# Kernel tuning notes

Hardware: AMD Instinct MI355X
Metric: run time of the kernel (lower is better)

Reference implementation:

```python
import jax, jax.numpy as jnp
import numpy as np

HEADS = 8

def setup_inputs() -> dict:
    key = jax.random.key(0)
    ks = jax.random.split(key, 10)
    B, C, D, W, H = 4, 256, 12, 12, 12
    dk = C // HEADS
    return {
        "x": jax.random.normal(ks[0], (B, C, D, W, H), jnp.float32),
        "wq": jax.random.normal(ks[1], (C, C), jnp.float32) * 0.05,
        "bq": jax.random.normal(ks[2], (C,), jnp.float32) * 0.05,
        "wk": jax.random.normal(ks[3], (C, C), jnp.float32) * 0.05,
        "bk": jax.random.normal(ks[4], (C,), jnp.float32) * 0.05,
        "wv": jax.random.normal(ks[5], (C, C), jnp.float32) * 0.05,
        "bv": jax.random.normal(ks[6], (C,), jnp.float32) * 0.05,
        "rel_d": jax.random.normal(ks[7], (1, HEADS, dk, D, 1, 1), jnp.float32),
        "rel_h": jax.random.normal(ks[8], (1, HEADS, dk, 1, 1, H), jnp.float32),
        "rel_w": jax.random.normal(ks[9], (1, HEADS, dk, 1, W, 1), jnp.float32),
    }


def reference(x, wq, bq, wk, bk, wv, bv, rel_d, rel_h, rel_w):
    B, C, D, W, H = x.shape
    dk = C // HEADS
    N = D * W * H

    def proj(w, b):
        # Conv3d kernel_size=1 == per-voxel linear over channels
        y = jnp.einsum('bcdwh,oc->bodwh', x, w) + b[None, :, None, None, None]
        return y.reshape(B, HEADS, dk, N)  # [B,h,dk,N]

    q = proj(wq, bq)
    k = proj(wk, bk)
    v = proj(wv, bv)

    # content-content: q^T k -> [B,h,N,N]
    cc = jnp.einsum('bhdn,bhdm->bhnm', q, k)
    # relative-position bias: (rel_h+rel_w+rel_d) broadcasts to [1,h,dk,D,W,H]
    pos = (rel_h + rel_w + rel_d).reshape(1, HEADS, dk, N)
    # content-position: pos^T @ q -> [B,h,N,N]
    cp = jnp.einsum('bhdn,bhdm->bhnm', pos, q)

    attn = jax.nn.softmax(cc + cp, axis=-1)  # [B,h,N,N]
    # out = v @ attn^T -> [B,h,dk,N]
    out = jnp.einsum('bhdn,bhmn->bhdm', v, attn)
    return out.reshape(B, C, D, W, H)
```

## Files before the change

### kernel.cpp

```cpp
#include <hip/hip_runtime.h>
#include <math.h>

#define HEADS 8
#define DK 32
#define B_ 4
#define C_ 256
#define NVOX 1728
#define DE 64
#define XPITCH 136
#define CPITCH 36
#define LOG2E 1.44269504088896f
#define JSPLIT 3
#define NJT 9
#define ITILES 14

typedef _Float16 f16x8 __attribute__((ext_vector_type(8)));
typedef __fp16 fp16x2 __attribute__((ext_vector_type(2)));
typedef float f32x16 __attribute__((ext_vector_type(16)));

__device__ inline float h2f(short s) {
    _Float16 h = *(_Float16*)&s;
    return (float)h;
}
__device__ inline f32x16 mfma32h(f16x8 a, f16x8 b, f32x16 c) {
    return __builtin_amdgcn_mfma_f32_32x32x16_f16(a, b, c, 0, 0, 0);
}
__device__ __forceinline__ void gl_lds16(const short* g, short* l) {
    __builtin_amdgcn_global_load_lds(
        (const __attribute__((address_space(1))) unsigned int*)g,
        (__attribute__((address_space(3))) unsigned int*)l, 16, 0, 0);
}

union H8 { _Float16 h[8]; uint4 v; };
union H4 { _Float16 h[4]; uint2 v; };
union PW { fp16x2 h2; unsigned int u; };

__global__ __launch_bounds__(256)
void prep_kernel(const float* __restrict__ x,
                 const float* __restrict__ wq, const float* __restrict__ wk,
                 const float* __restrict__ wv,
                 const float* __restrict__ rel_d, const float* __restrict__ rel_h,
                 const float* __restrict__ rel_w,
                 short* __restrict__ wf, short* __restrict__ xf,
                 short* __restrict__ Qf) {
    __shared__ float tile[64][65];
    int bid = blockIdx.x;
    int t = threadIdx.x;

    if (bid < 192) {
        int idx = (bid * 256 + t) * 4;
        int m = idx >> 16;
        const float* w = (m == 0) ? wq : (m == 1) ? wk : wv;
        float4 v = *(const float4*)&w[idx & 65535];
        H4 hh;
        hh.h[0] = (_Float16)v.x; hh.h[1] = (_Float16)v.y;
        hh.h[2] = (_Float16)v.z; hh.h[3] = (_Float16)v.w;
        *(uint2*)&wf[idx] = hh.v;
    } else if (bid < 624) {
        int q = bid - 192;
        int nb = (q % 27) * 64;
        int c0 = ((q / 27) % 4) * 64;
        int b  = q / 108;
        const float* xb = x + (size_t)b * C_ * NVOX;
        for (int e = t; e < 4096; e += 256) {
            int ci = e >> 6, nl = e & 63;
            tile[ci][nl] = xb[(size_t)(c0 + ci) * NVOX + nb + nl];
        }
        __syncthreads();
        for (int e = t; e < 512; e += 256) {
            int n = e >> 3, cg = (e & 7) * 8;
            H8 hi;
            #pragma unroll
            for (int j = 0; j < 8; j++) hi.h[j] = (_Float16)tile[cg + j][n];
            *(uint4*)&xf[((size_t)b * NVOX + nb + n) * C_ + c0 + cg] = hi.v;
        }
    } else {
        int q = bid - 624;
        int nb = (q % 27) * 64;
        int h  = (q / 27) % 8;
        int b  = q / 216;
        int bh = b * HEADS + h;
        int nl = t & 63, dd0 = (t >> 6) * 8;
        int n = nb + nl;
        int di = n / 144, wi = (n / 12) % 12, hi = n % 12;
        H8 ph;
        #pragma unroll
        for (int o = 0; o < 8; o++) {
            int hd = h * DK + dd0 + o;
            ph.h[o] = (_Float16)(rel_d[hd * 12 + di] + rel_w[hd * 12 + wi] +
                                 rel_h[hd * 12 + hi]);
        }
        *(uint4*)&Qf[((size_t)bh * NVOX + n) * DE + DK + dd0] = ph.v;
    }
}

struct FS {
    union {
        short xs[64 * XPITCH];
        float cbuf[3][64][CPITCH];
    } u;
};

__global__ __launch_bounds__(384, 4)
void fproj_kernel(const short* __restrict__ xf, const short* __restrict__ wf,
                  const float* __restrict__ bq, const float* __restrict__ bk,
                  const float* __restrict__ bv,
                  short* __restrict__ Qf, short* __restrict__ Kf,
                  short* __restrict__ Vf) {
    __shared__ FS sm;
    int nb = blockIdx.x * 64, h = blockIdx.y, b = blockIdx.z;
    int bh = b * HEADS + h;
    int t = threadIdx.x;
    int w = t >> 6, l = t & 63, ln = l & 31, hv = l >> 5;
    int mat = w >> 1, nh = w & 1;

    const short* xb = xf + ((size_t)b * NVOX + nb) * C_;
    const short* wA = wf + ((size_t)mat * C_ + h * DK + ln) * C_;
    int xrow = (nh * 32 + ln) * XPITCH;

    f32x16 acc;
    #pragma unroll
    for (int r = 0; r < 16; r++) acc[r] = 0.f;

    #pragma unroll 1
    for (int ch = 0; ch < 2; ch++) {
        __syncthreads();
        for (int e = t; e < 1024; e += 384) {
            int row = e >> 4, c8 = (e & 15) * 8;
            *(uint4*)&sm.u.xs[row * XPITCH + c8] =
                *(const uint4*)&xb[row * C_ + ch * 128 + c8];
        }
        __syncthreads();
        #pragma unroll 4
        for (int ks = 0; ks < 8; ks++) {
            int kl_ = ks * 16 + hv * 8;
            f16x8 a = *(const f16x8*)&wA[ch * 128 + kl_];
            f16x8 bfr = *(const f16x8*)&sm.u.xs[xrow + kl_];
            acc = mfma32h(a, bfr, acc);
        }
    }
    __syncthreads();

    const float* bias = (mat == 0) ? bq : (mat == 1) ? bk : bv;
    int ncol = nh * 32 + ln;
    #pragma unroll
    for (int q2 = 0; q2 < 4; q2++) {
        float4 cv;
        float* cvp = (float*)&cv;
        #pragma unroll
        for (int m = 0; m < 4; m++) {
            int o_loc = 8 * q2 + 4 * hv + m;
            cvp[m] = acc[4 * q2 + m] + bias[h * DK + o_loc];
        }
        *(float4*)&sm.u.cbuf[mat][ncol][8 * q2 + 4 * hv] = cv;
    }
    __syncthreads();

    if (t < 256) {
        int n = t >> 2, ddg = (t & 3) * 8;
        H8 qh, kh;
        #pragma unroll
        for (int j = 0; j < 8; j++) {
            qh.h[j] = (_Float16)sm.u.cbuf[0][n][ddg + j];
            kh.h[j] = (_Float16)sm.u.cbuf[1][n][ddg + j];
        }
        *(uint4*)&Qf[((size_t)bh * NVOX + nb + n) * DE + ddg] = qh.v;
        *(uint4*)&Kf[((size_t)bh * NVOX + nb + n) * DK + ddg] = kh.v;
    }
    if (t < 256) {
        int d = t >> 3, ng = (t & 7) * 8;
        H8 vv;
        #pragma unroll
        for (int j = 0; j < 8; j++)
            vv.h[j] = (_Float16)sm.u.cbuf[2][ng + j][d];
        *(uint4*)&Vf[((size_t)bh * DK + d) * NVOX + nb + ng] = vv.v;
    }
}

__global__ __launch_bounds__(256, 4)
void attn_kernel(const short* __restrict__ Qf, const short* __restrict__ Kf,
                 const short* __restrict__ Vf,
                 short* __restrict__ wsO, float* __restrict__ wsM,
                 float* __restrict__ wsL) {
    __shared__ __align__(16) short Ksm[2][4096];
    __shared__ __align__(16) short Vsm[2][2048];
    int id = blockIdx.x;
    int x8 = id & 7;
    int rr = id >> 3;
    int g  = rr / 42;
    int k_ = rr - g * 42;
    int bh = g * 8 + x8;
    int it = k_ / 3;
    int jp = k_ - it * 3;
    int t = threadIdx.x;
    int w  = t >> 6;
    int l  = t & 63;
    int ln = l & 31;
    int hv = l >> 5;
    int i_glob = it * 128 + w * 32 + ln;
    int iq = i_glob < NVOX ? i_glob : NVOX - 1;

    const short* Qp = Qf + (size_t)bh * NVOX * DE;
    const short* Kp = Kf + (size_t)bh * NVOX * DK;
    const short* Vp = Vf + (size_t)bh * DK * NVOX;

    f16x8 qf[4];
    #pragma unroll
    for (int ks = 0; ks < 4; ks++)
        qf[ks] = *(const f16x8*)&Qp[(size_t)iq * DE + ks * 16 + hv * 8];

    int jb0 = jp * NJT * 64;

    const short* gk0 = Kp + (size_t)(jb0 + (l ^ (w + 0))) * DK + (w + 0) * 8;
    const short* gk1 = Qp + (size_t)(jb0 + (l ^ (w + 4))) * DE + (w + 0) * 8;
    int vb0 = 2 * w + hv;
    const short* gv0 = Vp + (size_t)(ln ^ vb0) * NVOX + jb0 + vb0 * 8;

#define STAGE(bufp) do {                                   \
        short* kl_ = &Ksm[bufp][0];                        \
        short* vl_ = &Vsm[bufp][0];                        \
        gl_lds16(gk0, kl_ + (w + 0) * 512);                \
        gl_lds16(gk1, kl_ + (w + 4) * 512);                \
        gl_lds16(gv0, vl_ + (w + 0) * 512);                \
        gk0 += 64 * DK; gk1 += 64 * DE; gv0 += 64;         \
    } while (0)

    float mL = -INFINITY;
    float lsum = 0.f;
    f32x16 O;
    #pragma unroll
    for (int r = 0; r < 16; r++) O[r] = 0.f;

    STAGE(0);

    #pragma unroll 1
    for (int jt = 0; jt < NJT; ++jt) {
        int buf = jt & 1;
        __syncthreads();
        if (jt + 1 < NJT) STAGE(buf ^ 1);

        const short* Kb = &Ksm[buf][0];
        const short* Vb = &Vsm[buf][0];

        f32x16 sc[2];
        __builtin_amdgcn_s_setprio(1);
        #pragma unroll
        for (int js = 0; js < 2; js++) {
            f32x16 s;
            #pragma unroll
            for (int r = 0; r < 16; r++) s[r] = 0.f;
            #pragma unroll
            for (int ks = 0; ks < 4; ks++) {
                int kb = ks * 2 + hv;
                f16x8 kfr = *(const f16x8*)&Kb[kb * 512 + js * 256 + (ln ^ kb) * 8];
                s = mfma32h(kfr, qf[ks], s);
            }
            sc[js] = s;
        }
        __builtin_amdgcn_s_setprio(0);

        float m0 = fmaxf(sc[0][0], sc[1][0]);
        float m1 = fmaxf(sc[0][1], sc[1][1]);
        float m2 = fmaxf(sc[0][2], sc[1][2]);
        float m3 = fmaxf(sc[0][3], sc[1][3]);
        #pragma unroll
        for (int r = 4; r < 16; r += 4) {
            m0 = fmaxf(m0, fmaxf(sc[0][r + 0], sc[1][r + 0]));
            m1 = fmaxf(m1, fmaxf(sc[0][r + 1], sc[1][r + 1]));
            m2 = fmaxf(m2, fmaxf(sc[0][r + 2], sc[1][r + 2]));
            m3 = fmaxf(m3, fmaxf(sc[0][r + 3], sc[1][r + 3]));
        }
        float mx = fmaxf(fmaxf(m0, m1), fmaxf(m2, m3));
        mx = fmaxf(mx, __shfl_xor(mx, 32));
        float mxl = mx * LOG2E;
        if (!__all(mxl <= mL + 4.0f)) {
            float mLn = fmaxf(mL, mxl);
            float alpha = exp2f(mL - mLn);
            mL = mLn;
            lsum *= alpha;
            #pragma unroll
            for (int r = 0; r < 16; r++) O[r] *= alpha;
        }

        float ps0 = 0.f, ps1 = 0.f, ps2 = 0.f, ps3 = 0.f;
        #pragma unroll
        for (int js = 0; js < 2; js++) {
            #pragma unroll
            for (int r = 0; r < 16; r += 4) {
                float p0 = exp2f(fmaf(sc[js][r + 0], LOG2E, -mL));
                float p1 = exp2f(fmaf(sc[js][r + 1], LOG2E, -mL));
                float p2 = exp2f(fmaf(sc[js][r + 2], LOG2E, -mL));
                float p3 = exp2f(fmaf(sc[js][r + 3], LOG2E, -mL));
                sc[js][r + 0] = p0; sc[js][r + 1] = p1;
                sc[js][r + 2] = p2; sc[js][r + 3] = p3;
                ps0 += p0; ps1 += p1; ps2 += p2; ps3 += p3;
            }
        }
        float ps = (ps0 + ps1) + (ps2 + ps3);
        ps += __shfl_xor(ps, 32);
        lsum += ps;

        __builtin_amdgcn_s_setprio(1);
        #pragma unroll
        for (int ks = 0; ks < 4; ks++) {
            int js = ks >> 1, u8 = (ks & 1) * 8;
            PW a0p, a1p, b0p, b1p;
            a0p.h2 = __builtin_amdgcn_cvt_pkrtz(sc[js][u8 + 0], sc[js][u8 + 1]);
            a1p.h2 = __builtin_amdgcn_cvt_pkrtz(sc[js][u8 + 2], sc[js][u8 + 3]);
            b0p.h2 = __builtin_amdgcn_cvt_pkrtz(sc[js][u8 + 4], sc[js][u8 + 5]);
            b1p.h2 = __builtin_amdgcn_cvt_pkrtz(sc[js][u8 + 6], sc[js][u8 + 7]);
            auto r0 = __builtin_amdgcn_permlane32_swap(a0p.u, b0p.u, false, false);
            auto r1 = __builtin_amdgcn_permlane32_swap(a1p.u, b1p.u, false, false);
            union { unsigned int w4[4]; f16x8 f; } pb;
            pb.w4[0] = r0[0]; pb.w4[1] = r1[0];
            pb.w4[2] = r0[1]; pb.w4[3] = r1[1];
            int vb = ks * 2 + hv;
            f16x8 va = *(const f16x8*)&Vb[vb * 256 + (ln ^ vb) * 8];
            O = mfma32h(va, pb.f, O);
        }
        __builtin_amdgcn_s_setprio(0);
    }
#undef STAGE

    if (i_glob < NVOX) {
        short* Op = wsO + ((size_t)jp * (B_ * HEADS) + bh) * DK * NVOX;
        #pragma unroll
        for (int r = 0; r < 16; r++) {
            int d = (r & 3) + 8 * (r >> 2) + 4 * hv;
            _Float16 oh = (_Float16)O[r];
            Op[(size_t)d * NVOX + i_glob] = *(short*)&oh;
        }
        if (hv == 0) {
            size_t mo = ((size_t)jp * (B_ * HEADS) + bh) * NVOX + i_glob;
            wsM[mo] = mL;
            wsL[mo] = lsum;
        }
    }
}

__global__ void combine_kernel(const short* __restrict__ wsO,
                               const float* __restrict__ wsM,
                               const float* __restrict__ wsL,
                               float* __restrict__ out) {
    int idx = (blockIdx.x * 256 + threadIdx.x) * 4;
    int i = idx % NVOX;
    int bh = (idx / NVOX) >> 5;
    const size_t oh = (size_t)B_ * HEADS * DK * NVOX;
    const size_t mh = (size_t)B_ * HEADS * NVOX;
    size_t mo = (size_t)bh * NVOX + i;
    float4 m0 = *(const float4*)&wsM[mo];
    float4 m1 = *(const float4*)&wsM[mh + mo];
    float4 m2 = *(const float4*)&wsM[2 * mh + mo];
    float4 l0 = *(const float4*)&wsL[mo];
    float4 l1 = *(const float4*)&wsL[mh + mo];
    float4 l2 = *(const float4*)&wsL[2 * mh + mo];
    uint2 o0u = *(const uint2*)&wsO[idx];
    uint2 o1u = *(const uint2*)&wsO[oh + idx];
    uint2 o2u = *(const uint2*)&wsO[2 * oh + idx];
    const short* o0s = (const short*)&o0u;
    const short* o1s = (const short*)&o1u;
    const short* o2s = (const short*)&o2u;
    const float* m0p = (const float*)&m0; const float* m1p = (const float*)&m1;
    const float* m2p = (const float*)&m2;
    const float* l0p = (const float*)&l0; const float* l1p = (const float*)&l1;
    const float* l2p = (const float*)&l2;
    float4 res;
    float* rp = (float*)&res;
    #pragma unroll
    for (int j = 0; j < 4; j++) {
        float m = fmaxf(fmaxf(m0p[j], m1p[j]), m2p[j]);
        float a0 = exp2f(m0p[j] - m);
        float a1 = exp2f(m1p[j] - m);
        float a2 = exp2f(m2p[j] - m);
        rp[j] = (a0 * h2f(o0s[j]) + a1 * h2f(o1s[j]) + a2 * h2f(o2s[j])) /
                (a0 * l0p[j] + a1 * l1p[j] + a2 * l2p[j]);
    }
    *(float4*)&out[idx] = res;
}

extern "C" void kernel_launch(void* const* d_in, const int* in_sizes, int n_in,
                              void* d_out, int out_size, void* d_ws, size_t ws_size,
                              hipStream_t stream) {
    const float* x     = (const float*)d_in[0];
    const float* wq    = (const float*)d_in[1];
    const float* bq    = (const float*)d_in[2];
    const float* wk    = (const float*)d_in[3];
    const float* bk    = (const float*)d_in[4];
    const float* wv    = (const float*)d_in[5];
    const float* bv    = (const float*)d_in[6];
    const float* rel_d = (const float*)d_in[7];
    const float* rel_h = (const float*)d_in[8];
    const float* rel_w = (const float*)d_in[9];
    float* out = (float*)d_out;

    size_t qksz = (size_t)B_ * HEADS * NVOX * DE;
    size_t vsz  = (size_t)B_ * HEADS * DK * NVOX;
    short* Qf  = (short*)d_ws;
    short* Kf  = Qf + qksz;
    short* Vf  = Kf + vsz;
    short* wf  = Vf + vsz;
    short* wsO = wf + (size_t)3 * C_ * C_;
    float* wsM = (float*)(wsO + 3 * vsz);
    float* wsL = wsM + 3 * (size_t)B_ * HEADS * NVOX;
    short* xf  = wsO;

    prep_kernel<<<dim3(1488), dim3(256), 0, stream>>>(
        x, wq, wk, wv, rel_d, rel_h, rel_w, wf, xf, Qf);
    fproj_kernel<<<dim3(NVOX / 64, HEADS, B_), dim3(384), 0, stream>>>(
        xf, wf, bq, bk, bv, Qf, Kf, Vf);
    attn_kernel<<<dim3(ITILES * JSPLIT * HEADS * B_), dim3(256), 0, stream>>>(
        Qf, Kf, Vf, wsO, wsM, wsL);
    combine_kernel<<<dim3((int)(vsz / 1024)), dim3(256), 0, stream>>>(wsO, wsM, wsL, out);
}
```

Measured before the change: 153.1 us.

## Fuse fp16 conversion prep kernel into projection kernel

Removes the separate prep kernel that converted x and the weights to fp16 and wrote the positional half of Q. The projection kernel now reads fp32 x straight into LDS in channel-major layout, converts weights and activations to fp16 in registers, and computes the positional embedding itself. This saves a kernel launch and the round trip of the intermediate fp16 buffers. In exchange it loads twice as many bytes of x, redundantly reloads x for each of the 8 heads, does strided scalar LDS reads for the B fragment, and uses a larger LDS tile that may reduce occupancy.

```diff
diff --git a/kernel.cpp b/kernel.cpp
--- a/kernel.cpp
+++ b/kernel.cpp
@@ -7,7 +7,7 @@
 #define C_ 256
 #define NVOX 1728
 #define DE 64
-#define XPITCH 136
+#define XP32 66
 #define CPITCH 36
 #define LOG2E 1.44269504088896f
 #define JSPLIT 3
@@ -32,79 +32,23 @@
 }
 
 union H8 { _Float16 h[8]; uint4 v; };
-union H4 { _Float16 h[4]; uint2 v; };
 union PW { fp16x2 h2; unsigned int u; };
-
-__global__ __launch_bounds__(256)
-void prep_kernel(const float* __restrict__ x,
-                 const float* __restrict__ wq, const float* __restrict__ wk,
-                 const float* __restrict__ wv,
-                 const float* __restrict__ rel_d, const float* __restrict__ rel_h,
-                 const float* __restrict__ rel_w,
-                 short* __restrict__ wf, short* __restrict__ xf,
-                 short* __restrict__ Qf) {
-    __shared__ float tile[64][65];
-    int bid = blockIdx.x;
-    int t = threadIdx.x;
-
-    if (bid < 192) {
-        int idx = (bid * 256 + t) * 4;
-        int m = idx >> 16;
-        const float* w = (m == 0) ? wq : (m == 1) ? wk : wv;
-        float4 v = *(const float4*)&w[idx & 65535];
-        H4 hh;
-        hh.h[0] = (_Float16)v.x; hh.h[1] = (_Float16)v.y;
-        hh.h[2] = (_Float16)v.z; hh.h[3] = (_Float16)v.w;
-        *(uint2*)&wf[idx] = hh.v;
-    } else if (bid < 624) {
-        int q = bid - 192;
-        int nb = (q % 27) * 64;
-        int c0 = ((q / 27) % 4) * 64;
-        int b  = q / 108;
-        const float* xb = x + (size_t)b * C_ * NVOX;
-        for (int e = t; e < 4096; e += 256) {
-            int ci = e >> 6, nl = e & 63;
-            tile[ci][nl] = xb[(size_t)(c0 + ci) * NVOX + nb + nl];
-        }
-        __syncthreads();
-        for (int e = t; e < 512; e += 256) {
-            int n = e >> 3, cg = (e & 7) * 8;
-            H8 hi;
-            #pragma unroll
-            for (int j = 0; j < 8; j++) hi.h[j] = (_Float16)tile[cg + j][n];
-            *(uint4*)&xf[((size_t)b * NVOX + nb + n) * C_ + c0 + cg] = hi.v;
-        }
-    } else {
-        int q = bid - 624;
-        int nb = (q % 27) * 64;
-        int h  = (q / 27) % 8;
-        int b  = q / 216;
-        int bh = b * HEADS + h;
-        int nl = t & 63, dd0 = (t >> 6) * 8;
-        int n = nb + nl;
-        int di = n / 144, wi = (n / 12) % 12, hi = n % 12;
-        H8 ph;
-        #pragma unroll
-        for (int o = 0; o < 8; o++) {
-            int hd = h * DK + dd0 + o;
-            ph.h[o] = (_Float16)(rel_d[hd * 12 + di] + rel_w[hd * 12 + wi] +
-                                 rel_h[hd * 12 + hi]);
-        }
-        *(uint4*)&Qf[((size_t)bh * NVOX + n) * DE + DK + dd0] = ph.v;
-    }
-}
 
 struct FS {
     union {
-        short xs[64 * XPITCH];
+        float xs[128 * XP32];
         float cbuf[3][64][CPITCH];
     } u;
 };
 
 __global__ __launch_bounds__(384, 4)
-void fproj_kernel(const short* __restrict__ xf, const short* __restrict__ wf,
+void fproj_kernel(const float* __restrict__ x,
+                  const float* __restrict__ wq, const float* __restrict__ wk,
+                  const float* __restrict__ wv,
                   const float* __restrict__ bq, const float* __restrict__ bk,
                   const float* __restrict__ bv,
+                  const float* __restrict__ rel_d, const float* __restrict__ rel_h,
+                  const float* __restrict__ rel_w,
                   short* __restrict__ Qf, short* __restrict__ Kf,
                   short* __restrict__ Vf) {
     __shared__ FS sm;
@@ -114,9 +58,24 @@
     int w = t >> 6, l = t & 63, ln = l & 31, hv = l >> 5;
     int mat = w >> 1, nh = w & 1;
 
-    const short* xb = xf + ((size_t)b * NVOX + nb) * C_;
-    const short* wA = wf + ((size_t)mat * C_ + h * DK + ln) * C_;
-    int xrow = (nh * 32 + ln) * XPITCH;
+    if (t < 256) {
+        int n_ = t >> 2, dd0 = (t & 3) * 8;
+        int n = nb + n_;
+        int di = n / 144, wi = (n / 12) % 12, hi = n % 12;
+        H8 ph;
+        #pragma unroll
+        for (int o = 0; o < 8; o++) {
+            int hd = h * DK + dd0 + o;
+            ph.h[o] = (_Float16)(rel_d[hd * 12 + di] + rel_w[hd * 12 + wi] +
+                                 rel_h[hd * 12 + hi]);
+        }
+        *(uint4*)&Qf[((size_t)bh * NVOX + n) * DE + DK + dd0] = ph.v;
+    }
+
+    const float* wsrc = (mat == 0) ? wq : (mat == 1) ? wk : wv;
+    const float* wA = wsrc + (size_t)(h * DK + ln) * C_;
+    const float* xb = x + (size_t)b * C_ * NVOX + nb;
+    int col = nh * 32 + ln;
 
     f32x16 acc;
     #pragma unroll
@@ -125,24 +84,32 @@
     #pragma unroll 1
     for (int ch = 0; ch < 2; ch++) {
         __syncthreads();
-        for (int e = t; e < 1024; e += 384) {
-            int row = e >> 4, c8 = (e & 15) * 8;
-            *(uint4*)&sm.u.xs[row * XPITCH + c8] =
-                *(const uint4*)&xb[row * C_ + ch * 128 + c8];
+        for (int e = t; e < 4096; e += 384) {
+            int ci = e >> 5, n2 = (e & 31) * 2;
+            *(float2*)&sm.u.xs[ci * XP32 + n2] =
+                *(const float2*)&xb[(size_t)(ch * 128 + ci) * NVOX + n2];
         }
         __syncthreads();
         #pragma unroll 4
         for (int ks = 0; ks < 8; ks++) {
             int kl_ = ks * 16 + hv * 8;
-            f16x8 a = *(const f16x8*)&wA[ch * 128 + kl_];
-            f16x8 bfr = *(const f16x8*)&sm.u.xs[xrow + kl_];
-            acc = mfma32h(a, bfr, acc);
+            float4 w0 = *(const float4*)&wA[ch * 128 + kl_];
+            float4 w1 = *(const float4*)&wA[ch * 128 + kl_ + 4];
+            H8 ah;
+            ah.h[0] = (_Float16)w0.x; ah.h[1] = (_Float16)w0.y;
+            ah.h[2] = (_Float16)w0.z; ah.h[3] = (_Float16)w0.w;
+            ah.h[4] = (_Float16)w1.x; ah.h[5] = (_Float16)w1.y;
+            ah.h[6] = (_Float16)w1.z; ah.h[7] = (_Float16)w1.w;
+            H8 bh8;
+            #pragma unroll
+            for (int j = 0; j < 8; j++)
+                bh8.h[j] = (_Float16)sm.u.xs[(kl_ + j) * XP32 + col];
+            acc = mfma32h(*(const f16x8*)&ah, *(const f16x8*)&bh8, acc);
         }
     }
     __syncthreads();
 
     const float* bias = (mat == 0) ? bq : (mat == 1) ? bk : bv;
-    int ncol = nh * 32 + ln;
     #pragma unroll
     for (int q2 = 0; q2 < 4; q2++) {
         float4 cv;
@@ -152,7 +119,7 @@
             int o_loc = 8 * q2 + 4 * hv + m;
             cvp[m] = acc[4 * q2 + m] + bias[h * DK + o_loc];
         }
-        *(float4*)&sm.u.cbuf[mat][ncol][8 * q2 + 4 * hv] = cv;
+        *(float4*)&sm.u.cbuf[mat][col][8 * q2 + 4 * hv] = cv;
     }
     __syncthreads();
 
@@ -398,16 +365,12 @@
     short* Qf  = (short*)d_ws;
     short* Kf  = Qf + qksz;
     short* Vf  = Kf + vsz;
-    short* wf  = Vf + vsz;
-    short* wsO = wf + (size_t)3 * C_ * C_;
+    short* wsO = Vf + vsz;
     float* wsM = (float*)(wsO + 3 * vsz);
     float* wsL = wsM + 3 * (size_t)B_ * HEADS * NVOX;
-    short* xf  = wsO;
-
-    prep_kernel<<<dim3(1488), dim3(256), 0, stream>>>(
-        x, wq, wk, wv, rel_d, rel_h, rel_w, wf, xf, Qf);
+
     fproj_kernel<<<dim3(NVOX / 64, HEADS, B_), dim3(384), 0, stream>>>(
-        xf, wf, bq, bk, bv, Qf, Kf, Vf);
+        x, wq, wk, wv, bq, bk, bv, rel_d, rel_h, rel_w, Qf, Kf, Vf);
     attn_kernel<<<dim3(ITILES * JSPLIT * HEADS * B_), dim3(256), 0, stream>>>(
         Qf, Kf, Vf, wsO, wsM, wsL);
     combine_kernel<<<dim3((int)(vsz / 1024)), dim3(256), 0, stream>>>(wsO, wsM, wsL, out);
```

After: 171.2 us. 1.12x slower.

## Split attention KV tiles across two wave groups per block with in-block merge

Applied to the files above, without the earlier changes.

The attention block grows from 256 to 512 threads. Two groups of four waves each take part of the block's key/value tiles (5 and 4), each with its own double-buffered LDS staging. At the end, group 1 writes its partial O, max and sum to shared memory, and group 0 merges them with online-softmax rescaling before writing out. The aim is to shorten each block's serial KV loop and raise wave-level parallelism, at the cost of more LDS, an extra merge step and barriers that group 1 also waits on during its idle fifth iteration.

```diff
diff --git a/kernel.cpp b/kernel.cpp
--- a/kernel.cpp
+++ b/kernel.cpp
@@ -177,13 +177,14 @@
     }
 }
 
-__global__ __launch_bounds__(256, 4)
+struct AS { short K[2][4096]; short V[2][2048]; };
+
+__global__ __launch_bounds__(512, 4)
 void attn_kernel(const short* __restrict__ Qf, const short* __restrict__ Kf,
                  const short* __restrict__ Vf,
                  short* __restrict__ wsO, float* __restrict__ wsM,
                  float* __restrict__ wsL) {
-    __shared__ __align__(16) short Ksm[2][4096];
-    __shared__ __align__(16) short Vsm[2][2048];
+    __shared__ __align__(16) AS gsm[2];
     int id = blockIdx.x;
     int x8 = id & 7;
     int rr = id >> 3;
@@ -194,11 +195,16 @@
     int jp = k_ - it * 3;
     int t = threadIdx.x;
     int w  = t >> 6;
+    int grp = w >> 2;
+    int wl  = w & 3;
     int l  = t & 63;
     int ln = l & 31;
     int hv = l >> 5;
-    int i_glob = it * 128 + w * 32 + ln;
+    int i_glob = it * 128 + wl * 32 + ln;
     int iq = i_glob < NVOX ? i_glob : NVOX - 1;
+
+    int cnt   = grp ? 4 : 5;
+    int tile0 = grp ? 5 : 0;
 
     const short* Qp = Qf + (size_t)bh * NVOX * DE;
     const short* Kp = Kf + (size_t)bh * NVOX * DK;
@@ -209,19 +215,19 @@
     for (int ks = 0; ks < 4; ks++)
         qf[ks] = *(const f16x8*)&Qp[(size_t)iq * DE + ks * 16 + hv * 8];
 
-    int jb0 = jp * NJT * 64;
-
-    const short* gk0 = Kp + (size_t)(jb0 + (l ^ (w + 0))) * DK + (w + 0) * 8;
-    const short* gk1 = Qp + (size_t)(jb0 + (l ^ (w + 4))) * DE + (w + 0) * 8;
-    int vb0 = 2 * w + hv;
+    int jb0 = jp * NJT * 64 + tile0 * 64;
+
+    const short* gk0 = Kp + (size_t)(jb0 + (l ^ (wl + 0))) * DK + (wl + 0) * 8;
+    const short* gk1 = Qp + (size_t)(jb0 + (l ^ (wl + 4))) * DE + (wl + 0) * 8;
+    int vb0 = 2 * wl + hv;
     const short* gv0 = Vp + (size_t)(ln ^ vb0) * NVOX + jb0 + vb0 * 8;
 
 #define STAGE(bufp) do {                                   \
-        short* kl_ = &Ksm[bufp][0];                        \
-        short* vl_ = &Vsm[bufp][0];                        \
-        gl_lds16(gk0, kl_ + (w + 0) * 512);                \
-        gl_lds16(gk1, kl_ + (w + 4) * 512);                \
-        gl_lds16(gv0, vl_ + (w + 0) * 512);                \
+        short* kl_ = &gsm[grp].K[bufp][0];                 \
+        short* vl_ = &gsm[grp].V[bufp][0];                 \
+        gl_lds16(gk0, kl_ + (wl + 0) * 512);               \
+        gl_lds16(gk1, kl_ + (wl + 4) * 512);               \
+        gl_lds16(gv0, vl_ + (wl + 0) * 512);               \
         gk0 += 64 * DK; gk1 += 64 * DE; gv0 += 64;         \
     } while (0)
 
@@ -234,106 +240,123 @@
     STAGE(0);
 
     #pragma unroll 1
-    for (int jt = 0; jt < NJT; ++jt) {
-        int buf = jt & 1;
+    for (int s = 0; s < 5; ++s) {
+        int buf = s & 1;
         __syncthreads();
-        if (jt + 1 < NJT) STAGE(buf ^ 1);
-
-        const short* Kb = &Ksm[buf][0];
-        const short* Vb = &Vsm[buf][0];
-
-        f32x16 sc[2];
-        __builtin_amdgcn_s_setprio(1);
-        #pragma unroll
-        for (int js = 0; js < 2; js++) {
-            f32x16 s;
+        if (s + 1 < cnt) STAGE(buf ^ 1);
+        if (s < cnt) {
+            const short* Kb = &gsm[grp].K[buf][0];
+            const short* Vb = &gsm[grp].V[buf][0];
+
+            f32x16 sc[2];
+            __builtin_amdgcn_s_setprio(1);
             #pragma unroll
-            for (int r = 0; r < 16; r++) s[r] = 0.f;
+            for (int js = 0; js < 2; js++) {
+                f32x16 s_;
+                #pragma unroll
+                for (int r = 0; r < 16; r++) s_[r] = 0.f;
+                #pragma unroll
+                for (int ks = 0; ks < 4; ks++) {
+                    int kb = ks * 2 + hv;
+                    f16x8 kfr = *(const f16x8*)&Kb[kb * 512 + js * 256 + (ln ^ kb) * 8];
+                    s_ = mfma32h(kfr, qf[ks], s_);
+                }
+                sc[js] = s_;
+            }
+            __builtin_amdgcn_s_setprio(0);
+
+            float m0 = fmaxf(sc[0][0], sc[1][0]);
+            float m1 = fmaxf(sc[0][1], sc[1][1]);
+            float m2 = fmaxf(sc[0][2], sc[1][2]);
+            float m3 = fmaxf(sc[0][3], sc[1][3]);
+            #pragma unroll
+            for (int r = 4; r < 16; r += 4) {
+                m0 = fmaxf(m0, fmaxf(sc[0][r + 0], sc[1][r + 0]));
+                m1 = fmaxf(m1, fmaxf(sc[0][r + 1], sc[1][r + 1]));
+                m2 = fmaxf(m2, fmaxf(sc[0][r + 2], sc[1][r + 2]));
+                m3 = fmaxf(m3, fmaxf(sc[0][r + 3], sc[1][r + 3]));
+            }
+            float mx = fmaxf(fmaxf(m0, m1), fmaxf(m2, m3));
+            mx = fmaxf(mx, __shfl_xor(mx, 32));
+            float mxl = mx * LOG2E;
+            if (!__all(mxl <= mL + 4.0f)) {
+                float mLn = fmaxf(mL, mxl);
+                float alpha = exp2f(mL - mLn);
+                mL = mLn;
+                lsum *= alpha;
+                #pragma unroll
+                for (int r = 0; r < 16; r++) O[r] *= alpha;
+            }
+
+            float ps0 = 0.f, ps1 = 0.f, ps2 = 0.f, ps3 = 0.f;
+            #pragma unroll
+            for (int js = 0; js < 2; js++) {
+                #pragma unroll
+                for (int r = 0; r < 16; r += 4) {
+                    float p0 = exp2f(fmaf(sc[js][r + 0], LOG2E, -mL));
+                    float p1 = exp2f(fmaf(sc[js][r + 1], LOG2E, -mL));
+                    float p2 = exp2f(fmaf(sc[js][r + 2], LOG2E, -mL));
+                    float p3 = exp2f(fmaf(sc[js][r + 3], LOG2E, -mL));
+                    sc[js][r + 0] = p0; sc[js][r + 1] = p1;
+                    sc[js][r + 2] = p2; sc[js][r + 3] = p3;
+                    ps0 += p0; ps1 += p1; ps2 += p2; ps3 += p3;
+                }
+            }
+            float ps = (ps0 + ps1) + (ps2 + ps3);
+            ps += __shfl_xor(ps, 32);
+            lsum += ps;
+
+            __builtin_amdgcn_s_setprio(1);
             #pragma unroll
             for (int ks = 0; ks < 4; ks++) {
-                int kb = ks * 2 + hv;
-                f16x8 kfr = *(const f16x8*)&Kb[kb * 512 + js * 256 + (ln ^ kb) * 8];
-                s = mfma32h(kfr, qf[ks], s);
+                int js = ks >> 1, u8 = (ks & 1) * 8;
+                PW a0p, a1p, b0p, b1p;
+                a0p.h2 = __builtin_amdgcn_cvt_pkrtz(sc[js][u8 + 0], sc[js][u8 + 1]);
+                a1p.h2 = __builtin_amdgcn_cvt_pkrtz(sc[js][u8 + 2], sc[js][u8 + 3]);
+                b0p.h2 = __builtin_amdgcn_cvt_pkrtz(sc[js][u8 + 4], sc[js][u8 + 5]);
+                b1p.h2 = __builtin_amdgcn_cvt_pkrtz(sc[js][u8 + 6], sc[js][u8 + 7]);
+                auto r0 = __builtin_amdgcn_permlane32_swap(a0p.u, b0p.u, false, false);
+                auto r1 = __builtin_amdgcn_permlane32_swap(a1p.u, b1p.u, false, false);
+                union { unsigned int w4[4]; f16x8 f; } pb;
+                pb.w4[0] = r0[0]; pb.w4[1] = r1[0];
+                pb.w4[2] = r0[1]; pb.w4[3] = r1[1];
+                int vb = ks * 2 + hv;
+                f16x8 va = *(const f16x8*)&Vb[vb * 256 + (ln ^ vb) * 8];
+                O = mfma32h(va, pb.f, O);
             }
-            sc[js] = s;
-        }
-        __builtin_amdgcn_s_setprio(0);
-
-        float m0 = fmaxf(sc[0][0], sc[1][0]);
-        float m1 = fmaxf(sc[0][1], sc[1][1]);
-        float m2 = fmaxf(sc[0][2], sc[1][2]);
-        float m3 = fmaxf(sc[0][3], sc[1][3]);
-        #pragma unroll
-        for (int r = 4; r < 16; r += 4) {
-            m0 = fmaxf(m0, fmaxf(sc[0][r + 0], sc[1][r + 0]));
-            m1 = fmaxf(m1, fmaxf(sc[0][r + 1], sc[1][r + 1]));
-            m2 = fmaxf(m2, fmaxf(sc[0][r + 2], sc[1][r + 2]));
-            m3 = fmaxf(m3, fmaxf(sc[0][r + 3], sc[1][r + 3]));
-        }
-        float mx = fmaxf(fmaxf(m0, m1), fmaxf(m2, m3));
-        mx = fmaxf(mx, __shfl_xor(mx, 32));
-        float mxl = mx * LOG2E;
-        if (!__all(mxl <= mL + 4.0f)) {
-            float mLn = fmaxf(mL, mxl);
-            float alpha = exp2f(mL - mLn);
-            mL = mLn;
-            lsum *= alpha;
-            #pragma unroll
-            for (int r = 0; r < 16; r++) O[r] *= alpha;
-        }
-
-        float ps0 = 0.f, ps1 = 0.f, ps2 = 0.f, ps3 = 0.f;
-        #pragma unroll
-        for (int js = 0; js < 2; js++) {
-            #pragma unroll
-            for (int r = 0; r < 16; r += 4) {
-                float p0 = exp2f(fmaf(sc[js][r + 0], LOG2E, -mL));
-                float p1 = exp2f(fmaf(sc[js][r + 1], LOG2E, -mL));
-                float p2 = exp2f(fmaf(sc[js][r + 2], LOG2E, -mL));
-                float p3 = exp2f(fmaf(sc[js][r + 3], LOG2E, -mL));
-                sc[js][r + 0] = p0; sc[js][r + 1] = p1;
-                sc[js][r + 2] = p2; sc[js][r + 3] = p3;
-                ps0 += p0; ps1 += p1; ps2 += p2; ps3 += p3;
-            }
-        }
-        float ps = (ps0 + ps1) + (ps2 + ps3);
-        ps += __shfl_xor(ps, 32);
-        lsum += ps;
-
-        __builtin_amdgcn_s_setprio(1);
-        #pragma unroll
-        for (int ks = 0; ks < 4; ks++) {
-            int js = ks >> 1, u8 = (ks & 1) * 8;
-            PW a0p, a1p, b0p, b1p;
-            a0p.h2 = __builtin_amdgcn_cvt_pkrtz(sc[js][u8 + 0], sc[js][u8 + 1]);
-            a1p.h2 = __builtin_amdgcn_cvt_pkrtz(sc[js][u8 + 2], sc[js][u8 + 3]);
-            b0p.h2 = __builtin_amdgcn_cvt_pkrtz(sc[js][u8 + 4], sc[js][u8 + 5]);
-            b1p.h2 = __builtin_amdgcn_cvt_pkrtz(sc[js][u8 + 6], sc[js][u8 + 7]);
-            auto r0 = __builtin_amdgcn_permlane32_swap(a0p.u, b0p.u, false, false);
-            auto r1 = __builtin_amdgcn_permlane32_swap(a1p.u, b1p.u, false, false);
-            union { unsigned int w4[4]; f16x8 f; } pb;
-            pb.w4[0] = r0[0]; pb.w4[1] = r1[0];
-            pb.w4[2] = r0[1]; pb.w4[3] = r1[1];
-            int vb = ks * 2 + hv;
-            f16x8 va = *(const f16x8*)&Vb[vb * 256 + (ln ^ vb) * 8];
-            O = mfma32h(va, pb.f, O);
-        }
-        __builtin_amdgcn_s_setprio(0);
+            __builtin_amdgcn_s_setprio(0);
+        }
     }
 #undef STAGE
 
-    if (i_glob < NVOX) {
+    __syncthreads();
+    float* mb = (float*)&gsm[0];
+    int sl = wl * 64 + l;
+    if (grp == 1) {
+        #pragma unroll
+        for (int r = 0; r < 16; r++) mb[sl * 17 + r] = O[r];
+        mb[4400 + sl] = mL;
+        mb[4700 + sl] = lsum;
+    }
+    __syncthreads();
+    if (grp == 0 && i_glob < NVOX) {
+        float m1 = mb[4400 + sl];
+        float l1 = mb[4700 + sl];
+        float mm = fmaxf(mL, m1);
+        float a0 = exp2f(mL - mm);
+        float a1 = exp2f(m1 - mm);
+        float lq = lsum * a0 + l1 * a1;
         short* Op = wsO + ((size_t)jp * (B_ * HEADS) + bh) * DK * NVOX;
         #pragma unroll
         for (int r = 0; r < 16; r++) {
             int d = (r & 3) + 8 * (r >> 2) + 4 * hv;
-            _Float16 oh = (_Float16)O[r];
+            _Float16 oh = (_Float16)(O[r] * a0 + mb[sl * 17 + r] * a1);
             Op[(size_t)d * NVOX + i_glob] = *(short*)&oh;
         }
         if (hv == 0) {
             size_t mo = ((size_t)jp * (B_ * HEADS) + bh) * NVOX + i_glob;
-            wsM[mo] = mL;
-            wsL[mo] = lsum;
+            wsM[mo] = mm;
+            wsL[mo] = lq;
         }
     }
 }
@@ -408,7 +431,7 @@
         x, wq, wk, wv, rel_d, rel_h, rel_w, wf, xf, Qf);
     fproj_kernel<<<dim3(NVOX / 64, HEADS, B_), dim3(384), 0, stream>>>(
         xf, wf, bq, bk, bv, Qf, Kf, Vf);
-    attn_kernel<<<dim3(ITILES * JSPLIT * HEADS * B_), dim3(256), 0, stream>>>(
+    attn_kernel<<<dim3(ITILES * JSPLIT * HEADS * B_), dim3(512), 0, stream>>>(
         Qf, Kf, Vf, wsO, wsM, wsL);
     combine_kernel<<<dim3((int)(vsz / 1024)), dim3(256), 0, stream>>>(wsO, wsM, wsL, out);
 }
```

Measured after the change: 153.8 us. About the same (+0.5%).
